# Kernel tuning notes

Measured on AMD Instinct MI355X. Metric: run time of the kernel, lower is better.

Reference implementation:

```python
import math
import jax, jax.numpy as jnp
import numpy as np

D, N, B, L = 1024, 16, 8, 4096
SCALE = math.sqrt(1.0 / float(N))


def setup_inputs() -> dict:
    key = jax.random.key(0)
    ks = jax.random.split(key, 8)
    x = jax.random.normal(ks[0], (B, D, L), dtype=jnp.float32)
    p_logit = 0.2 * jax.random.normal(ks[1], (D, N), dtype=jnp.float32)
    # reset_parameters(): radius = 1 - sigmoid(p_logit) * delta, phases evenly spaced
    delta = jax.nn.sigmoid(0.2 * jax.random.normal(ks[2], (D, N), dtype=jnp.float32))
    freqs = jnp.exp(jnp.arange(1, D + 1, dtype=jnp.float32) * (-math.log(D) / float(D)))
    freqs = jax.random.permutation(ks[3], freqs)[:, None]            # (D,1)
    theta = freqs * (2.0 * math.pi / float(N))
    phi = theta * jnp.arange(1, N + 1, dtype=jnp.float32)[None, :]   # (D,N)
    p = jax.nn.sigmoid(p_logit)
    radius = 1.0 - p * delta                                         # in (0,1)
    log_q_real = jnp.log(radius)
    log_q_imag = phi
    gamma_real = jax.random.normal(ks[4], (D, N), dtype=jnp.float32)
    gamma_imag = jnp.zeros((D, N), dtype=jnp.float32)
    omega = 0.25 * jax.random.truncated_normal(ks[5], -4.0, 4.0, (D,), dtype=jnp.float32)
    return {"x": x, "p_logit": p_logit, "log_q_real": log_q_real,
            "log_q_imag": log_q_imag, "gamma_real": gamma_real,
            "gamma_imag": gamma_imag, "omega": omega}


def reference(x, p_logit, log_q_real, log_q_imag, gamma_real, gamma_imag, omega):
    # FFT path (hx=None, compute_last_state=False)
    p = jax.nn.sigmoid(p_logit).astype(jnp.float32)                  # (D,N)
    log_q = jax.lax.complex(log_q_real, log_q_imag)                  # complex64 (D,N)
    gamma = jax.lax.complex(gamma_real, gamma_imag) * SCALE          # (D,N)
    t = jnp.arange(L, dtype=jnp.float32)
    # q^t = exp(t * log_q)  (== cumprod of q in the torch code)
    q_pows = jnp.exp(log_q[:, :, None] * t[None, None, :])           # (D,N,L) complex64
    kernel = jnp.einsum('dn,dnl->dl', gamma * p.astype(gamma.dtype), q_pows)  # (D,L)
    fft_len = 1 << int(2 * L - 1).bit_length()
    X = jnp.fft.fft(x.astype(jnp.complex64), n=fft_len, axis=-1)     # (B,D,F)
    K = jnp.fft.fft(kernel, n=fft_len, axis=-1)                      # (D,F)
    y = jnp.fft.ifft(X * K[None], axis=-1)[..., :L].real.astype(x.dtype)
    residual = x * omega[None, :, None]
    return y + residual
```

## Files before the change

### kernel.cpp

```cpp
#include <hip/hip_runtime.h>
#include <hip/hip_bf16.h>
#include <math.h>

#define D_DIM   1024
#define NM      16
#define B_DIM   8
#define L_DIM   4096
#define SCALE_F 0.25f
#define NK      5
#define WPB     4
#define TPW     4
#define NITER   4
#define LBUF    2560

typedef __attribute__((ext_vector_type(8))) short bf16x8;
typedef __attribute__((ext_vector_type(4))) float f32x4;

union U4 { uint4 u; bf16x8 v; };

__device__ __forceinline__ unsigned rot16(unsigned v) { return (v >> 16) | (v << 16); }
__device__ __forceinline__ unsigned short f2bf(float f) {
    __hip_bfloat16 h = __float2bfloat16(f);
    return *reinterpret_cast<unsigned short*>(&h);
}
__device__ __forceinline__ float bflo(unsigned u) { return __uint_as_float(u << 16); }
__device__ __forceinline__ float bfhi(unsigned u) { return __uint_as_float(u & 0xffff0000u); }
__device__ __forceinline__ int swz(int a) { return a ^ (((a >> 7) & 7) << 4); }

__global__ __launch_bounds__(256)
void ema_mkA(const float* __restrict__ p_logit, const float* __restrict__ lqr,
             const float* __restrict__ lqi, const float* __restrict__ gr,
             const float* __restrict__ gi, uint4* __restrict__ wsa)
{
    const int wid  = blockIdx.x * WPB + (threadIdx.x >> 6);
    const int lane = threadIdx.x & 63;
    const int d    = wid / NK;
    const int k    = wid - d * NK;
    const int i    = lane & 15, g = lane >> 4;
    const int t0   = i - 15 + 32 * k + 8 * g;
    const float t0f = (float)t0;

    float acc[8];
#pragma unroll
    for (int e = 0; e < 8; ++e) acc[e] = 0.0f;

#pragma unroll 1
    for (int n = 0; n < NM; ++n) {
        const int idx = d * NM + n;
        const float pp = 1.0f / (1.0f + __expf(-p_logit[idx]));
        const float CR = gr[idx] * (SCALE_F * pp);
        const float CI = gi[idx] * (SCALE_F * pp);
        const float LR = lqr[idx], LI = lqi[idx];

        float sq, cq; __sincosf(LI, &sq, &cq);
        const float eq = __expf(LR);
        const float qr = eq * cq, qi = eq * sq;
        float s0, c0; __sincosf(t0f * LI, &s0, &c0);
        const float e0 = __expf(t0f * LR);
        float wr = e0 * c0, wi = e0 * s0;

#pragma unroll
        for (int e = 0; e < 8; ++e) {
            acc[e] = fmaf(CR, wr, fmaf(-CI, wi, acc[e]));
            const float nwr = fmaf(wr, qr, -wi * qi);
            const float nwi = fmaf(wr, qi,  wi * qr);
            wr = nwr; wi = nwi;
        }
    }

    unsigned pk[4];
#pragma unroll
    for (int e = 0; e < 8; ++e) {
        const unsigned b = (t0 + e >= 0) ? (unsigned)f2bf(acc[e]) : 0u;
        if ((e & 1) == 0) pk[e >> 1] = b; else pk[e >> 1] |= b << 16;
    }
    wsa[(size_t)(d * NK + k) * 64 + lane] = make_uint4(pk[0], pk[1], pk[2], pk[3]);
}

__device__ void compute_afrag(int d, int lane,
                              const float* __restrict__ p_logit,
                              const float* __restrict__ lqr,
                              const float* __restrict__ lqi,
                              const float* __restrict__ gr,
                              const float* __restrict__ gi,
                              bf16x8 (&af)[NK])
{
    float LR[NM], LI[NM], CR[NM], CI[NM];
#pragma unroll
    for (int n = 0; n < NM; ++n) {
        const int idx = d * NM + n;
        const float p = 1.0f / (1.0f + __expf(-p_logit[idx]));
        LR[n] = lqr[idx]; LI[n] = lqi[idx];
        CR[n] = gr[idx] * (SCALE_F * p);
        CI[n] = gi[idx] * (SCALE_F * p);
    }
    const int i = lane & 15, g = lane >> 4;
#pragma unroll
    for (int k = 0; k < NK; ++k) {
        unsigned pk[4] = {0, 0, 0, 0};
#pragma unroll
        for (int e = 0; e < 8; ++e) {
            const int t = i - 15 + 32 * k + 8 * g + e;
            float v = 0.0f;
            if (t >= 0) {
                const float tf = (float)t;
#pragma unroll
                for (int n = 0; n < NM; ++n) {
                    const float er = __expf(tf * LR[n]);
                    float s, c; __sincosf(tf * LI[n], &s, &c);
                    v += er * fmaf(CR[n], c, -CI[n] * s);
                }
            }
            const unsigned b = f2bf(v);
            if ((e & 1) == 0) pk[e >> 1] = b; else pk[e >> 1] |= b << 16;
        }
        U4 u; u.u = make_uint4(pk[0], pk[1], pk[2], pk[3]); af[k] = u.v;
    }
}

template<bool FROM_WS>
__global__ __launch_bounds__(256)
void ema_fir(const float* __restrict__ x,
             const float* __restrict__ p_logit,
             const float* __restrict__ lqr, const float* __restrict__ lqi,
             const float* __restrict__ gr, const float* __restrict__ gi,
             const float* __restrict__ omega,
             const uint4* __restrict__ wsa,
             float* __restrict__ out)
{
    __shared__ __align__(16) char smem[WPB][2][LBUF];

    const int w    = threadIdx.x >> 6;
    const int lane = threadIdx.x & 63;
    const int wid  = blockIdx.x * WPB + w;
    const int d    = wid >> 3;
    const int sub  = wid & 7;
    const int qtr  = sub & 3;
    const int bgrp = sub >> 2;
    const int j    = lane & 15, g = lane >> 4;

    const size_t rstride = (size_t)D_DIM * L_DIM;
    const float* xcol = x   + (size_t)(bgrp * 4 * D_DIM + d) * L_DIM + qtr * 1024;
    float*       ycol = out + (size_t)(bgrp * 4 * D_DIM + d) * L_DIM + qtr * 1024;

    const float om = omega[d];

    bf16x8 af[NK];
    if (FROM_WS) {
#pragma unroll
        for (int k = 0; k < NK; ++k) {
            U4 u; u.u = wsa[(size_t)(d * NK + k) * 64 + lane];
            af[k] = u.v;
        }
    } else {
        compute_afrag(d, lane, p_logit, lqr, lqi, gr, gi, af);
    }

    float4 c4 = make_float4(0.f, 0.f, 0.f, 0.f);
    if (qtr != 0)
        c4 = *reinterpret_cast<const float4*>(xcol - 256 + lane * 4);
    float4 r[4];
#pragma unroll
    for (int v = 0; v < 4; ++v)
        r[v] = *reinterpret_cast<const float4*>(xcol + lane * 16 + 4 * v);

#pragma unroll 1
    for (int i = 0; i < NITER; ++i) {
        char* sb = smem[w][i & 1];

        {
            uint2 cpk;
            cpk.x = (unsigned)f2bf(c4.x) | ((unsigned)f2bf(c4.y) << 16);
            cpk.y = (unsigned)f2bf(c4.z) | ((unsigned)f2bf(c4.w) << 16);
            *reinterpret_cast<uint2*>(sb + swz(lane * 8)) = cpk;

            unsigned pk[8];
#pragma unroll
            for (int v = 0; v < 4; ++v) {
                pk[2 * v + 0] = (unsigned)f2bf(r[v].x) | ((unsigned)f2bf(r[v].y) << 16);
                pk[2 * v + 1] = (unsigned)f2bf(r[v].z) | ((unsigned)f2bf(r[v].w) << 16);
            }
            const int wbase = 512 + lane * 32;
            *reinterpret_cast<uint4*>(sb + swz(wbase))      = make_uint4(pk[0], pk[1], pk[2], pk[3]);
            *reinterpret_cast<uint4*>(sb + swz(wbase + 16)) = make_uint4(pk[4], pk[5], pk[6], pk[7]);
        }

        if (i < NITER - 1) {
            const float* xn = xcol + (size_t)(i + 1) * rstride;
            if (qtr != 0)
                c4 = *reinterpret_cast<const float4*>(xn - 256 + lane * 4);
#pragma unroll
            for (int v = 0; v < 4; ++v)
                r[v] = *reinterpret_cast<const float4*>(xn + lane * 16 + 4 * v);
        }

        float* yb = ycol + (size_t)i * rstride;
#pragma unroll
        for (int tt = 0; tt < TPW; ++tt) {
            f32x4 acc = {0.0f, 0.0f, 0.0f, 0.0f};
#pragma unroll
            for (int k = 0; k < NK; ++k) {
                const int boff = 512 * tt + 528 + 32 * j - 64 * k - 16 * g;
                U4 z; z.u = *reinterpret_cast<const uint4*>(sb + swz(boff));
                uint4 rv;
                rv.x = rot16(z.u.w); rv.y = rot16(z.u.z);
                rv.z = rot16(z.u.y); rv.w = rot16(z.u.x);
                U4 bfv; bfv.u = rv;
                acc = __builtin_amdgcn_mfma_f32_16x16x32_bf16(af[k], bfv.v, acc, 0, 0, 0);
            }
            const int lx = 512 * tt + 512 + 32 * j + 8 * g;
            const uint2 z2 = *reinterpret_cast<const uint2*>(sb + swz(lx));
            acc.x = fmaf(om, bflo(z2.x), acc.x);
            acc.y = fmaf(om, bfhi(z2.x), acc.y);
            acc.z = fmaf(om, bflo(z2.y), acc.z);
            acc.w = fmaf(om, bfhi(z2.y), acc.w);
            __builtin_nontemporal_store(acc,
                reinterpret_cast<f32x4*>(yb + tt * 256 + 16 * j + 4 * g));
        }
    }
}

extern "C" void kernel_launch(void* const* d_in, const int* in_sizes, int n_in,
                              void* d_out, int out_size, void* d_ws, size_t ws_size,
                              hipStream_t stream)
{
    const float* x   = (const float*)d_in[0];
    const float* pl  = (const float*)d_in[1];
    const float* lqr = (const float*)d_in[2];
    const float* lqi = (const float*)d_in[3];
    const float* gr  = (const float*)d_in[4];
    const float* gi  = (const float*)d_in[5];
    const float* om  = (const float*)d_in[6];
    float* out = (float*)d_out;

    const size_t needA = (size_t)D_DIM * NK * 64 * 16;
    dim3 grid((D_DIM * 8) / WPB), block(64 * WPB);

    if (ws_size >= needA) {
        ema_mkA<<<dim3(D_DIM * NK / WPB), dim3(64 * WPB), 0, stream>>>(
            pl, lqr, lqi, gr, gi, (uint4*)d_ws);
        ema_fir<true><<<grid, block, 0, stream>>>(x, pl, lqr, lqi, gr, gi, om,
                                                  (const uint4*)d_ws, out);
    } else {
        ema_fir<false><<<grid, block, 0, stream>>>(x, pl, lqr, lqi, gr, gi, om,
                                                   nullptr, out);
    }
}
```

Measured before the change: 59.68 us.

## Fuse kernel-coefficient generation into FIR kernel with block-shared row staging

Drops the separate coefficient-generation launch and its workspace round trip. Each block now covers one channel and batch group across the full sequence, and its four warps build the five MFMA A-fragments cooperatively into shared memory (warp 0 builds the fifth). The whole 4096-sample row is staged into a shared double buffer, so the warps no longer reload the overlapping halo from global memory. In exchange it adds block-wide barriers and per-block coefficient recomputation, which is imbalanced across warps, and the grid shrinks to 2048 blocks.

```diff
diff --git a/kernel.cpp b/kernel.cpp
--- a/kernel.cpp
+++ b/kernel.cpp
@@ -8,10 +8,8 @@
 #define L_DIM   4096
 #define SCALE_F 0.25f
 #define NK      5
-#define WPB     4
-#define TPW     4
 #define NITER   4
-#define LBUF    2560
+#define SROW    9216
 
 typedef __attribute__((ext_vector_type(8))) short bf16x8;
 typedef __attribute__((ext_vector_type(4))) float f32x4;
@@ -27,17 +25,16 @@
 __device__ __forceinline__ float bfhi(unsigned u) { return __uint_as_float(u & 0xffff0000u); }
 __device__ __forceinline__ int swz(int a) { return a ^ (((a >> 7) & 7) << 4); }
 
-__global__ __launch_bounds__(256)
-void ema_mkA(const float* __restrict__ p_logit, const float* __restrict__ lqr,
-             const float* __restrict__ lqi, const float* __restrict__ gr,
-             const float* __restrict__ gi, uint4* __restrict__ wsa)
+__device__ void compute_af_k(int d, int lane, int k,
+                             const float* __restrict__ p_logit,
+                             const float* __restrict__ lqr,
+                             const float* __restrict__ lqi,
+                             const float* __restrict__ gr,
+                             const float* __restrict__ gi,
+                             char* __restrict__ afb)
 {
-    const int wid  = blockIdx.x * WPB + (threadIdx.x >> 6);
-    const int lane = threadIdx.x & 63;
-    const int d    = wid / NK;
-    const int k    = wid - d * NK;
-    const int i    = lane & 15, g = lane >> 4;
-    const int t0   = i - 15 + 32 * k + 8 * g;
+    const int i = lane & 15, g = lane >> 4;
+    const int t0 = i - 15 + 32 * k + 8 * g;
     const float t0f = (float)t0;
 
     float acc[8];
@@ -74,133 +71,86 @@
         const unsigned b = (t0 + e >= 0) ? (unsigned)f2bf(acc[e]) : 0u;
         if ((e & 1) == 0) pk[e >> 1] = b; else pk[e >> 1] |= b << 16;
     }
-    wsa[(size_t)(d * NK + k) * 64 + lane] = make_uint4(pk[0], pk[1], pk[2], pk[3]);
-}
-
-__device__ void compute_afrag(int d, int lane,
-                              const float* __restrict__ p_logit,
-                              const float* __restrict__ lqr,
-                              const float* __restrict__ lqi,
-                              const float* __restrict__ gr,
-                              const float* __restrict__ gi,
-                              bf16x8 (&af)[NK])
+    *reinterpret_cast<uint4*>(afb + k * 1024 + lane * 16) =
+        make_uint4(pk[0], pk[1], pk[2], pk[3]);
+}
+
+__global__ __launch_bounds__(256)
+void ema_fused(const float* __restrict__ x,
+               const float* __restrict__ p_logit,
+               const float* __restrict__ lqr, const float* __restrict__ lqi,
+               const float* __restrict__ gr, const float* __restrict__ gi,
+               const float* __restrict__ omega,
+               float* __restrict__ out)
 {
-    float LR[NM], LI[NM], CR[NM], CI[NM];
-#pragma unroll
-    for (int n = 0; n < NM; ++n) {
-        const int idx = d * NM + n;
-        const float p = 1.0f / (1.0f + __expf(-p_logit[idx]));
-        LR[n] = lqr[idx]; LI[n] = lqi[idx];
-        CR[n] = gr[idx] * (SCALE_F * p);
-        CI[n] = gi[idx] * (SCALE_F * p);
-    }
-    const int i = lane & 15, g = lane >> 4;
+    __shared__ __align__(16) char sstage[2][SROW];
+    __shared__ __align__(16) char safb[NK * 1024];
+
+    const int tid  = threadIdx.x;
+    const int w    = tid >> 6;
+    const int lane = tid & 63;
+    const int bid  = blockIdx.x;
+    const int d    = bid >> 1;
+    const int bgrp = bid & 1;
+    const int j    = lane & 15, g = lane >> 4;
+
+    const size_t rstride = (size_t)D_DIM * L_DIM;
+    const float* xrow0 = x   + (size_t)(bgrp * 4 * D_DIM + d) * L_DIM;
+    float*       yrow0 = out + (size_t)(bgrp * 4 * D_DIM + d) * L_DIM;
+    const float  om    = omega[d];
+
+    if (tid < 64) {
+        const int h = tid & 31, buf = tid >> 5;
+        *reinterpret_cast<uint4*>(sstage[buf] + swz(h * 16)) =
+            make_uint4(0u, 0u, 0u, 0u);
+    }
+
+    float4 r[4];
+#pragma unroll
+    for (int v = 0; v < 4; ++v)
+        r[v] = *reinterpret_cast<const float4*>(xrow0 + tid * 16 + 4 * v);
+
+    compute_af_k(d, lane, w, p_logit, lqr, lqi, gr, gi, safb);
+    if (w == 0)
+        compute_af_k(d, lane, 4, p_logit, lqr, lqi, gr, gi, safb);
+
+    __syncthreads();
+
+    bf16x8 af[NK];
 #pragma unroll
     for (int k = 0; k < NK; ++k) {
-        unsigned pk[4] = {0, 0, 0, 0};
-#pragma unroll
-        for (int e = 0; e < 8; ++e) {
-            const int t = i - 15 + 32 * k + 8 * g + e;
-            float v = 0.0f;
-            if (t >= 0) {
-                const float tf = (float)t;
-#pragma unroll
-                for (int n = 0; n < NM; ++n) {
-                    const float er = __expf(tf * LR[n]);
-                    float s, c; __sincosf(tf * LI[n], &s, &c);
-                    v += er * fmaf(CR[n], c, -CI[n] * s);
-                }
-            }
-            const unsigned b = f2bf(v);
-            if ((e & 1) == 0) pk[e >> 1] = b; else pk[e >> 1] |= b << 16;
-        }
-        U4 u; u.u = make_uint4(pk[0], pk[1], pk[2], pk[3]); af[k] = u.v;
-    }
-}
-
-template<bool FROM_WS>
-__global__ __launch_bounds__(256)
-void ema_fir(const float* __restrict__ x,
-             const float* __restrict__ p_logit,
-             const float* __restrict__ lqr, const float* __restrict__ lqi,
-             const float* __restrict__ gr, const float* __restrict__ gi,
-             const float* __restrict__ omega,
-             const uint4* __restrict__ wsa,
-             float* __restrict__ out)
-{
-    __shared__ __align__(16) char smem[WPB][2][LBUF];
-
-    const int w    = threadIdx.x >> 6;
-    const int lane = threadIdx.x & 63;
-    const int wid  = blockIdx.x * WPB + w;
-    const int d    = wid >> 3;
-    const int sub  = wid & 7;
-    const int qtr  = sub & 3;
-    const int bgrp = sub >> 2;
-    const int j    = lane & 15, g = lane >> 4;
-
-    const size_t rstride = (size_t)D_DIM * L_DIM;
-    const float* xcol = x   + (size_t)(bgrp * 4 * D_DIM + d) * L_DIM + qtr * 1024;
-    float*       ycol = out + (size_t)(bgrp * 4 * D_DIM + d) * L_DIM + qtr * 1024;
-
-    const float om = omega[d];
-
-    bf16x8 af[NK];
-    if (FROM_WS) {
-#pragma unroll
-        for (int k = 0; k < NK; ++k) {
-            U4 u; u.u = wsa[(size_t)(d * NK + k) * 64 + lane];
-            af[k] = u.v;
-        }
-    } else {
-        compute_afrag(d, lane, p_logit, lqr, lqi, gr, gi, af);
-    }
-
-    float4 c4 = make_float4(0.f, 0.f, 0.f, 0.f);
-    if (qtr != 0)
-        c4 = *reinterpret_cast<const float4*>(xcol - 256 + lane * 4);
-    float4 r[4];
+        U4 u; u.u = *reinterpret_cast<const uint4*>(safb + k * 1024 + lane * 16);
+        af[k] = u.v;
+    }
+
+    {
+        unsigned pk[8];
+#pragma unroll
+        for (int v = 0; v < 4; ++v) {
+            pk[2 * v + 0] = (unsigned)f2bf(r[v].x) | ((unsigned)f2bf(r[v].y) << 16);
+            pk[2 * v + 1] = (unsigned)f2bf(r[v].z) | ((unsigned)f2bf(r[v].w) << 16);
+        }
+        const int wb = 512 + tid * 32;
+        *reinterpret_cast<uint4*>(sstage[0] + swz(wb))      = make_uint4(pk[0], pk[1], pk[2], pk[3]);
+        *reinterpret_cast<uint4*>(sstage[0] + swz(wb + 16)) = make_uint4(pk[4], pk[5], pk[6], pk[7]);
+    }
 #pragma unroll
     for (int v = 0; v < 4; ++v)
-        r[v] = *reinterpret_cast<const float4*>(xcol + lane * 16 + 4 * v);
+        r[v] = *reinterpret_cast<const float4*>(xrow0 + rstride + tid * 16 + 4 * v);
+
+    __syncthreads();
 
 #pragma unroll 1
     for (int i = 0; i < NITER; ++i) {
-        char* sb = smem[w][i & 1];
-
-        {
-            uint2 cpk;
-            cpk.x = (unsigned)f2bf(c4.x) | ((unsigned)f2bf(c4.y) << 16);
-            cpk.y = (unsigned)f2bf(c4.z) | ((unsigned)f2bf(c4.w) << 16);
-            *reinterpret_cast<uint2*>(sb + swz(lane * 8)) = cpk;
-
-            unsigned pk[8];
-#pragma unroll
-            for (int v = 0; v < 4; ++v) {
-                pk[2 * v + 0] = (unsigned)f2bf(r[v].x) | ((unsigned)f2bf(r[v].y) << 16);
-                pk[2 * v + 1] = (unsigned)f2bf(r[v].z) | ((unsigned)f2bf(r[v].w) << 16);
-            }
-            const int wbase = 512 + lane * 32;
-            *reinterpret_cast<uint4*>(sb + swz(wbase))      = make_uint4(pk[0], pk[1], pk[2], pk[3]);
-            *reinterpret_cast<uint4*>(sb + swz(wbase + 16)) = make_uint4(pk[4], pk[5], pk[6], pk[7]);
-        }
-
-        if (i < NITER - 1) {
-            const float* xn = xcol + (size_t)(i + 1) * rstride;
-            if (qtr != 0)
-                c4 = *reinterpret_cast<const float4*>(xn - 256 + lane * 4);
-#pragma unroll
-            for (int v = 0; v < 4; ++v)
-                r[v] = *reinterpret_cast<const float4*>(xn + lane * 16 + 4 * v);
-        }
-
-        float* yb = ycol + (size_t)i * rstride;
-#pragma unroll
-        for (int tt = 0; tt < TPW; ++tt) {
+        const char* sb = sstage[i & 1];
+        float* yb = yrow0 + (size_t)i * rstride + w * 1024;
+
+#pragma unroll
+        for (int tt = 0; tt < 4; ++tt) {
             f32x4 acc = {0.0f, 0.0f, 0.0f, 0.0f};
 #pragma unroll
             for (int k = 0; k < NK; ++k) {
-                const int boff = 512 * tt + 528 + 32 * j - 64 * k - 16 * g;
+                const int boff = 2048 * w + 512 * tt + 528 + 32 * j - 64 * k - 16 * g;
                 U4 z; z.u = *reinterpret_cast<const uint4*>(sb + swz(boff));
                 uint4 rv;
                 rv.x = rot16(z.u.w); rv.y = rot16(z.u.z);
@@ -208,7 +158,7 @@
                 U4 bfv; bfv.u = rv;
                 acc = __builtin_amdgcn_mfma_f32_16x16x32_bf16(af[k], bfv.v, acc, 0, 0, 0);
             }
-            const int lx = 512 * tt + 512 + 32 * j + 8 * g;
+            const int lx = 2048 * w + 512 * tt + 512 + 32 * j + 8 * g;
             const uint2 z2 = *reinterpret_cast<const uint2*>(sb + swz(lx));
             acc.x = fmaf(om, bflo(z2.x), acc.x);
             acc.y = fmaf(om, bfhi(z2.x), acc.y);
@@ -216,6 +166,27 @@
             acc.w = fmaf(om, bfhi(z2.y), acc.w);
             __builtin_nontemporal_store(acc,
                 reinterpret_cast<f32x4*>(yb + tt * 256 + 16 * j + 4 * g));
+        }
+
+        if (i < NITER - 1) {
+            char* nb = sstage[(i + 1) & 1];
+            unsigned pk[8];
+#pragma unroll
+            for (int v = 0; v < 4; ++v) {
+                pk[2 * v + 0] = (unsigned)f2bf(r[v].x) | ((unsigned)f2bf(r[v].y) << 16);
+                pk[2 * v + 1] = (unsigned)f2bf(r[v].z) | ((unsigned)f2bf(r[v].w) << 16);
+            }
+            const int wb = 512 + tid * 32;
+            *reinterpret_cast<uint4*>(nb + swz(wb))      = make_uint4(pk[0], pk[1], pk[2], pk[3]);
+            *reinterpret_cast<uint4*>(nb + swz(wb + 16)) = make_uint4(pk[4], pk[5], pk[6], pk[7]);
+
+            if (i < NITER - 2) {
+#pragma unroll
+                for (int v = 0; v < 4; ++v)
+                    r[v] = *reinterpret_cast<const float4*>(
+                        xrow0 + (size_t)(i + 2) * rstride + tid * 16 + 4 * v);
+            }
+            __syncthreads();
         }
     }
 }
@@ -233,16 +204,6 @@
     const float* om  = (const float*)d_in[6];
     float* out = (float*)d_out;
 
-    const size_t needA = (size_t)D_DIM * NK * 64 * 16;
-    dim3 grid((D_DIM * 8) / WPB), block(64 * WPB);
-
-    if (ws_size >= needA) {
-        ema_mkA<<<dim3(D_DIM * NK / WPB), dim3(64 * WPB), 0, stream>>>(
-            pl, lqr, lqi, gr, gi, (uint4*)d_ws);
-        ema_fir<true><<<grid, block, 0, stream>>>(x, pl, lqr, lqi, gr, gi, om,
-                                                  (const uint4*)d_ws, out);
-    } else {
-        ema_fir<false><<<grid, block, 0, stream>>>(x, pl, lqr, lqi, gr, gi, om,
-                                                   nullptr, out);
-    }
-}
+    dim3 grid(D_DIM * 2), block(256);
+    ema_fused<<<grid, block, 0, stream>>>(x, pl, lqr, lqi, gr, gi, om, out);
+}
```

Measured after the change: 52.85 us. -11.4%, faster.
